# Optimization experiments

Hardware: AMD Instinct MI355X
Metric: run time of the kernel (lower is better)

Reference implementation:

```python
import jax, jax.numpy as jnp
import numpy as np
from jax import lax

NUM_MARKETS = 32
WINDOW = 16
T = 1048576


def setup_inputs() -> dict:
    key = jax.random.key(0)
    k1, k2, k3, k4 = jax.random.split(key, 4)
    std = float(np.sqrt(WINDOW))  # matches nn.init.normal_(.., 0, sqrt(window_size))
    x = jax.random.normal(k1, (1, NUM_MARKETS, T), dtype=jnp.float32)
    start_pos = -jnp.ones((NUM_MARKETS, 1), dtype=jnp.float32)  # default start_pos = -1
    conv_w = jax.random.normal(k2, (NUM_MARKETS, NUM_MARKETS, WINDOW), dtype=jnp.float32) * std
    conv_b = jax.random.normal(k3, (NUM_MARKETS,), dtype=jnp.float32) * 0.05
    pos_weight = jax.random.normal(k4, (NUM_MARKETS, 1), dtype=jnp.float32) * std
    return {"x": x, "start_pos": start_pos, "conv_w": conv_w, "conv_b": conv_b, "pos_weight": pos_weight}


def reference(x, start_pos, conv_w, conv_b, pos_weight):
    # Conv1d, valid padding: [1, N, T] -> [1, N, L], L = T - WINDOW + 1
    y = lax.conv_general_dilated(
        x, conv_w, window_strides=(1,), padding="VALID",
        dimension_numbers=("NCH", "OIH", "NCH"),
    ) + conv_b[None, :, None]
    seq = y[0].T  # [L, N] time-major for the scan
    pw = pos_weight[:, 0]  # [N]

    def step(pos, xt):
        a = jnp.tanh(pos * pw + xt)  # [N]
        return jnp.sign(a), a

    _, outs = lax.scan(step, start_pos[:, 0], seq)  # outs: [L, N]
    positions = jnp.concatenate([start_pos, outs.T], axis=1)  # [N, L+1]
    return positions[None]  # [1, N, L+1]
```

## Files before the change

kernel.cpp:

```cpp
#include <hip/hip_runtime.h>
#include <stdint.h>

#define T_LEN    1048576
#define TY_LEN   1048561
#define OUT_W    1048562
#define NM       32
#define WIN      16
#define NCH      4096
#define CL       256
#define CBT      256
#define TPB      256
#define XS_W     272
#define NF4      68
#define YS_W     257

__device__ inline float sgnf(float a){
    return (a > 0.0f) ? 1.0f : ((a < 0.0f) ? -1.0f : 0.0f);
}

__device__ inline uint32_t map_comp(uint32_t f, uint32_t g){
    uint32_t r = 0;
#pragma unroll
    for (int k = 0; k < 4; ++k) {
        const uint32_t s = (g >> (8 * k)) & 0xFFu;
        const uint32_t o = (f >> (8 * s)) & 0xFFu;
        r |= o << (8 * k);
    }
    return r;
}

__global__ void wtrans_kernel(const float* __restrict__ w, float* __restrict__ wT2){
    const int idx = blockIdx.x * 256 + threadIdx.x;
    if (idx >= NM * NM * WIN) return;
    const int o = idx / (NM * WIN);
    const int r = idx - o * (NM * WIN);
    const int i = r / WIN;
    const int h = r - i * WIN;
    wT2[(((h * 4) + (o >> 3)) * NM + i) * 8 + (o & 7)] = w[idx];
}

__global__ __launch_bounds__(256, 4) void conv_kernel(
    const float* __restrict__ x, const float* __restrict__ wT2,
    const float* __restrict__ b, const float* __restrict__ sp,
    const float* __restrict__ pwv, float* __restrict__ out,
    uint32_t* __restrict__ trans)
{
    __shared__ float xs[NM * XS_W];
    __shared__ uint32_t maps8[NM * 8];
    const int base = blockIdx.x * TPB;
    for (int idx = threadIdx.x; idx < NM * NF4; idx += CBT) {
        const int i = idx / NF4;
        const int q = idx - i * NF4;
        const int t0 = base + q * 4;
        float4 v;
        if (t0 + 3 < T_LEN) {
            v = *reinterpret_cast<const float4*>(x + (size_t)i * T_LEN + t0);
        } else {
            v.x = (t0 + 0 < T_LEN) ? x[(size_t)i * T_LEN + t0 + 0] : 0.0f;
            v.y = (t0 + 1 < T_LEN) ? x[(size_t)i * T_LEN + t0 + 1] : 0.0f;
            v.z = (t0 + 2 < T_LEN) ? x[(size_t)i * T_LEN + t0 + 2] : 0.0f;
            v.w = (t0 + 3 < T_LEN) ? x[(size_t)i * T_LEN + t0 + 3] : 0.0f;
        }
        *reinterpret_cast<float4*>(&xs[i * XS_W + q * 4]) = v;
    }
    __syncthreads();
    const int lane = threadIdx.x & 63;
    const int og   = __builtin_amdgcn_readfirstlane(threadIdx.x >> 6);
    float acc[8][4];
#pragma unroll
    for (int oi = 0; oi < 8; ++oi)
#pragma unroll
        for (int tt = 0; tt < 4; ++tt) acc[oi][tt] = 0.0f;
#pragma unroll 1
    for (int h = 0; h < WIN; ++h) {
        const float* wp = wT2 + (size_t)(h * 4 + og) * (NM * 8);
#pragma unroll 1
        for (int c = 0; c < 4; ++c) {
            float xv[8][4];
#pragma unroll
            for (int i2 = 0; i2 < 8; ++i2) {
                const int i = c * 8 + i2;
#pragma unroll
                for (int tt = 0; tt < 4; ++tt)
                    xv[i2][tt] = xs[i * XS_W + lane + 64 * tt + h];
            }
#pragma unroll
            for (int i2 = 0; i2 < 8; ++i2) {
                const float* wr = wp + (c * 8 + i2) * 8;
#pragma unroll
                for (int oi = 0; oi < 8; ++oi) {
                    const float wv = wr[oi];
#pragma unroll
                    for (int tt = 0; tt < 4; ++tt)
                        acc[oi][tt] = fmaf(wv, xv[i2][tt], acc[oi][tt]);
                }
            }
        }
    }
    float yv[8][4];
    __syncthreads();
#pragma unroll
    for (int oi = 0; oi < 8; ++oi) {
        const int o = og * 8 + oi;
        const float bv = b[o];
#pragma unroll
        for (int tt = 0; tt < 4; ++tt) {
            yv[oi][tt] = acc[oi][tt] + bv;
            xs[o * YS_W + lane + 64 * tt] = yv[oi][tt];
        }
    }
    __syncthreads();
#pragma unroll
    for (int oi = 0; oi < 8; ++oi) {
        const int o = og * 8 + oi;
        float* orow = out + (size_t)o * OUT_W + 1 + base + lane;
#pragma unroll
        for (int tt = 0; tt < 4; ++tt) {
            const int t = base + lane + 64 * tt;
            if (t < TY_LEN) orow[64 * tt] = yv[oi][tt];
        }
    }
    {
        const int sm = threadIdx.x >> 3;
        const int ss = threadIdx.x & 7;
        const float pws = pwv[sm];
        float q0 = -1.0f, q1 = 0.0f, q2 = 1.0f, q3 = sp[sm];
        const int rem = TY_LEN - base;
        int st = rem - ss * 32; st = st < 0 ? 0 : (st > 32 ? 32 : st);
        const float* yr = &xs[sm * YS_W + ss * 32];
        for (int j = 0; j < st; ++j) {
            const float hv = yr[j];
            q0 = sgnf(fmaf(q0, pws, hv));
            q1 = sgnf(fmaf(q1, pws, hv));
            q2 = sgnf(fmaf(q2, pws, hv));
            q3 = sgnf(fmaf(q3, pws, hv));
        }
        const uint32_t e0 = (uint32_t)((int)q0 + 1);
        const uint32_t e1 = (uint32_t)((int)q1 + 1);
        const uint32_t e2 = (uint32_t)((int)q2 + 1);
        const uint32_t e3 = (st == 0) ? 3u : (uint32_t)((int)q3 + 1);
        maps8[sm * 8 + ss] = e0 | (e1 << 8) | (e2 << 16) | (e3 << 24);
    }
    __syncthreads();
    if (threadIdx.x < NM) {
        uint32_t seg = 0x03020100u;
#pragma unroll
        for (int s = 0; s < 8; ++s)
            seg = map_comp(maps8[threadIdx.x * 8 + s], seg);
        trans[threadIdx.x * NCH + blockIdx.x] = seg;
    }
}

__global__ __launch_bounds__(256) void scan_pass_b(
    const uint32_t* __restrict__ trans, uint8_t* __restrict__ entries)
{
    const uint32_t ID = 0x03020100u;
    const int m = blockIdx.x;
    const int tid = threadIdx.x;
    __shared__ uint32_t S[256];
    uint32_t maps[16];
    uint32_t seg = ID;
    const uint32_t* tr = trans + m * NCH + tid * 16;
#pragma unroll
    for (int j = 0; j < 16; ++j) { maps[j] = tr[j]; seg = map_comp(maps[j], seg); }
    S[tid] = seg;
    __syncthreads();
    for (int off = 1; off < 256; off <<= 1) {
        const uint32_t v = (tid >= off) ? S[tid - off] : ID;
        __syncthreads();
        if (tid >= off) S[tid] = map_comp(S[tid], v);
        __syncthreads();
    }
    const uint32_t pre = (tid == 0) ? ID : S[tid - 1];
    uint32_t s = (pre >> 24) & 0xFFu;
    uint8_t* er = entries + m * NCH + tid * 16;
#pragma unroll
    for (int j = 0; j < 16; ++j) {
        er[j] = (uint8_t)s;
        s = (maps[j] >> (8 * s)) & 0xFFu;
    }
}

__global__ __launch_bounds__(256) void scan_pass_c(
    float* yo, const float* __restrict__ sp, const float* __restrict__ pwv,
    const uint8_t* __restrict__ entries)
{
    const int gid = blockIdx.x * 256 + threadIdx.x;
    const int m = gid >> 12;
    const int c = gid & (NCH - 1);
    const float pw = pwv[m];
    const float spv = sp[m];
    const uint32_t s = entries[m * NCH + c];
    float p = (s == 3u) ? spv : ((float)(int)s - 1.0f);
    float* row = yo + (size_t)m * OUT_W + 1 + c * CL;
    if (c == 0) yo[(size_t)m * OUT_W] = spv;
    const int limit0 = TY_LEN - c * CL;
    const int limit = limit0 < CL ? limit0 : CL;
    int j = 0;
    for (; j + 4 <= limit; j += 4) {
        const float4 h = *reinterpret_cast<const float4*>(row + j);
        float a;
        a = fmaf(p, pw, h.x); row[j+0] = tanhf(a); p = sgnf(a);
        a = fmaf(p, pw, h.y); row[j+1] = tanhf(a); p = sgnf(a);
        a = fmaf(p, pw, h.z); row[j+2] = tanhf(a); p = sgnf(a);
        a = fmaf(p, pw, h.w); row[j+3] = tanhf(a); p = sgnf(a);
    }
    for (; j < limit; ++j) {
        const float a = fmaf(p, pw, row[j]);
        row[j] = tanhf(a);
        p = sgnf(a);
    }
}

extern "C" void kernel_launch(void* const* d_in, const int* in_sizes, int n_in,
                              void* d_out, int out_size, void* d_ws, size_t ws_size,
                              hipStream_t stream)
{
    const float* x   = (const float*)d_in[0];
    const float* spv = (const float*)d_in[1];
    const float* w   = (const float*)d_in[2];
    const float* b   = (const float*)d_in[3];
    const float* pw  = (const float*)d_in[4];
    float* out = (float*)d_out;

    uint8_t* ws = (uint8_t*)d_ws;
    float*    wT2     = (float*)ws;
    uint32_t* trans   = (uint32_t*)(ws + 65536);
    uint8_t*  entries = (uint8_t*)(ws + 65536 + 524288);

    wtrans_kernel<<<64, 256, 0, stream>>>(w, wT2);
    conv_kernel<<<NCH, CBT, 0, stream>>>(x, wT2, b, spv, pw, out, trans);
    scan_pass_b<<<NM, 256, 0, stream>>>(trans, entries);
    scan_pass_c<<<(NM * NCH) / 256, 256, 0, stream>>>(out, spv, pw, entries);
}
```

Measured before the change: 501.4 us.

## Refine scan granularity to 32-step chunks for more parallel fixup

The sign-recurrence scan now works on 32-element chunks instead of 256-element chunks. Each conv block writes its eight per-subchunk transition maps straight to global memory instead of composing them in shared memory. The final tanh pass then runs 8x more threads, each with a short serial chain of 32 steps, which shortens its critical path. In exchange, scan_pass_b must compose 128 maps per thread serially with global loads, and the transition and entry buffers grow 8x. The shared-memory staging layout also changes to 33-float padded rows to avoid bank conflicts.

```diff
diff --git a/kernel.cpp b/kernel.cpp
--- a/kernel.cpp
+++ b/kernel.cpp
@@ -6,13 +6,11 @@
 #define OUT_W    1048562
 #define NM       32
 #define WIN      16
-#define NCH      4096
-#define CL       256
+#define NCH32    32768
 #define CBT      256
 #define TPB      256
 #define XS_W     272
 #define NF4      68
-#define YS_W     257
 
 __device__ inline float sgnf(float a){
     return (a > 0.0f) ? 1.0f : ((a < 0.0f) ? -1.0f : 0.0f);
@@ -46,7 +44,6 @@
     uint32_t* __restrict__ trans)
 {
     __shared__ float xs[NM * XS_W];
-    __shared__ uint32_t maps8[NM * 8];
     const int base = blockIdx.x * TPB;
     for (int idx = threadIdx.x; idx < NM * NF4; idx += CBT) {
         const int i = idx / NF4;
@@ -106,7 +103,8 @@
 #pragma unroll
         for (int tt = 0; tt < 4; ++tt) {
             yv[oi][tt] = acc[oi][tt] + bv;
-            xs[o * YS_W + lane + 64 * tt] = yv[oi][tt];
+            const int sub = (lane >> 5) + 2 * tt;
+            xs[(o * 8 + sub) * 33 + (lane & 31)] = yv[oi][tt];
         }
     }
     __syncthreads();
@@ -125,9 +123,9 @@
         const int ss = threadIdx.x & 7;
         const float pws = pwv[sm];
         float q0 = -1.0f, q1 = 0.0f, q2 = 1.0f, q3 = sp[sm];
-        const int rem = TY_LEN - base;
-        int st = rem - ss * 32; st = st < 0 ? 0 : (st > 32 ? 32 : st);
-        const float* yr = &xs[sm * YS_W + ss * 32];
+        int st = TY_LEN - base - ss * 32;
+        st = st < 0 ? 0 : (st > 32 ? 32 : st);
+        const float* yr = &xs[(sm * 8 + ss) * 33];
         for (int j = 0; j < st; ++j) {
             const float hv = yr[j];
             q0 = sgnf(fmaf(q0, pws, hv));
@@ -139,15 +137,8 @@
         const uint32_t e1 = (uint32_t)((int)q1 + 1);
         const uint32_t e2 = (uint32_t)((int)q2 + 1);
         const uint32_t e3 = (st == 0) ? 3u : (uint32_t)((int)q3 + 1);
-        maps8[sm * 8 + ss] = e0 | (e1 << 8) | (e2 << 16) | (e3 << 24);
-    }
-    __syncthreads();
-    if (threadIdx.x < NM) {
-        uint32_t seg = 0x03020100u;
-#pragma unroll
-        for (int s = 0; s < 8; ++s)
-            seg = map_comp(maps8[threadIdx.x * 8 + s], seg);
-        trans[threadIdx.x * NCH + blockIdx.x] = seg;
+        trans[(size_t)sm * NCH32 + blockIdx.x * 8 + ss] =
+            e0 | (e1 << 8) | (e2 << 16) | (e3 << 24);
     }
 }
 
@@ -158,11 +149,9 @@
     const int m = blockIdx.x;
     const int tid = threadIdx.x;
     __shared__ uint32_t S[256];
-    uint32_t maps[16];
+    const uint32_t* tr = trans + (size_t)m * NCH32 + tid * 128;
     uint32_t seg = ID;
-    const uint32_t* tr = trans + m * NCH + tid * 16;
-#pragma unroll
-    for (int j = 0; j < 16; ++j) { maps[j] = tr[j]; seg = map_comp(maps[j], seg); }
+    for (int j = 0; j < 128; ++j) seg = map_comp(tr[j], seg);
     S[tid] = seg;
     __syncthreads();
     for (int off = 1; off < 256; off <<= 1) {
@@ -173,11 +162,10 @@
     }
     const uint32_t pre = (tid == 0) ? ID : S[tid - 1];
     uint32_t s = (pre >> 24) & 0xFFu;
-    uint8_t* er = entries + m * NCH + tid * 16;
-#pragma unroll
-    for (int j = 0; j < 16; ++j) {
+    uint8_t* er = entries + (size_t)m * NCH32 + tid * 128;
+    for (int j = 0; j < 128; ++j) {
         er[j] = (uint8_t)s;
-        s = (maps[j] >> (8 * s)) & 0xFFu;
+        s = (tr[j] >> (8 * s)) & 0xFFu;
     }
 }
 
@@ -186,29 +174,32 @@
     const uint8_t* __restrict__ entries)
 {
     const int gid = blockIdx.x * 256 + threadIdx.x;
-    const int m = gid >> 12;
-    const int c = gid & (NCH - 1);
+    const int m = gid >> 15;
+    const int c = gid & (NCH32 - 1);
     const float pw = pwv[m];
     const float spv = sp[m];
-    const uint32_t s = entries[m * NCH + c];
+    const uint32_t s = entries[(size_t)m * NCH32 + c];
     float p = (s == 3u) ? spv : ((float)(int)s - 1.0f);
-    float* row = yo + (size_t)m * OUT_W + 1 + c * CL;
+    float* row = yo + (size_t)m * OUT_W + 1 + (size_t)c * 32;
     if (c == 0) yo[(size_t)m * OUT_W] = spv;
-    const int limit0 = TY_LEN - c * CL;
-    const int limit = limit0 < CL ? limit0 : CL;
-    int j = 0;
-    for (; j + 4 <= limit; j += 4) {
-        const float4 h = *reinterpret_cast<const float4*>(row + j);
-        float a;
-        a = fmaf(p, pw, h.x); row[j+0] = tanhf(a); p = sgnf(a);
-        a = fmaf(p, pw, h.y); row[j+1] = tanhf(a); p = sgnf(a);
-        a = fmaf(p, pw, h.z); row[j+2] = tanhf(a); p = sgnf(a);
-        a = fmaf(p, pw, h.w); row[j+3] = tanhf(a); p = sgnf(a);
-    }
-    for (; j < limit; ++j) {
-        const float a = fmaf(p, pw, row[j]);
-        row[j] = tanhf(a);
-        p = sgnf(a);
+    const int limit0 = TY_LEN - c * 32;
+    const int limit = limit0 < 32 ? limit0 : 32;
+    if (limit == 32) {
+#pragma unroll
+        for (int j = 0; j < 32; j += 4) {
+            const float4 h = *reinterpret_cast<const float4*>(row + j);
+            float a;
+            a = fmaf(p, pw, h.x); row[j+0] = tanhf(a); p = sgnf(a);
+            a = fmaf(p, pw, h.y); row[j+1] = tanhf(a); p = sgnf(a);
+            a = fmaf(p, pw, h.z); row[j+2] = tanhf(a); p = sgnf(a);
+            a = fmaf(p, pw, h.w); row[j+3] = tanhf(a); p = sgnf(a);
+        }
+    } else {
+        for (int j = 0; j < limit; ++j) {
+            const float a = fmaf(p, pw, row[j]);
+            row[j] = tanhf(a);
+            p = sgnf(a);
+        }
     }
 }
 
@@ -226,10 +217,10 @@
     uint8_t* ws = (uint8_t*)d_ws;
     float*    wT2     = (float*)ws;
     uint32_t* trans   = (uint32_t*)(ws + 65536);
-    uint8_t*  entries = (uint8_t*)(ws + 65536 + 524288);
+    uint8_t*  entries = (uint8_t*)(ws + 65536 + (size_t)NM * NCH32 * 4);
 
     wtrans_kernel<<<64, 256, 0, stream>>>(w, wT2);
-    conv_kernel<<<NCH, CBT, 0, stream>>>(x, wT2, b, spv, pw, out, trans);
+    conv_kernel<<<4096, CBT, 0, stream>>>(x, wT2, b, spv, pw, out, trans);
     scan_pass_b<<<NM, 256, 0, stream>>>(trans, entries);
-    scan_pass_c<<<(NM * NCH) / 256, 256, 0, stream>>>(out, spv, pw, entries);
-}
+    scan_pass_c<<<(NM * NCH32) / 256, 256, 0, stream>>>(out, spv, pw, entries);
+}
```

Result: slower. 529.8 us (+5.6%).
